# Kernel tuning notes

Measured on AMD Instinct MI355X. Metric: run time of the kernel, lower is better.

The kernel has to match this reference:

```python
import jax, jax.numpy as jnp
import numpy as np

B, S, D = 4, 2048, 1024          # batch, seq, hidden_units
E, K, I = 16, 2, 1024            # n_routed_experts, top_k, moe_inter_dim
SH = 2                            # n_shared_experts -> shared inter = SH*I
ROUTE_SCALE = 1.0


def setup_inputs() -> dict:
    key = jax.random.key(0)
    ks = jax.random.split(key, 12)
    std = 0.02
    return {
        "x": jax.random.normal(ks[0], (B, S, D), jnp.float32),
        "gate_w": jax.random.normal(ks[1], (E, D), jnp.float32) * std,
        # expert weights, torch Linear layout [out, in], stacked over experts
        "w1": jax.random.normal(ks[2], (E, I, D), jnp.float32) * std,
        "w2": jax.random.normal(ks[3], (E, D, I), jnp.float32) * std,
        "w3": jax.random.normal(ks[4], (E, I, D), jnp.float32) * std,
        # shared expert MLP (bias=True, nn.Linear default)
        "sw1": jax.random.normal(ks[5], (SH * I, D), jnp.float32) * std,
        "sb1": jnp.zeros((SH * I,), jnp.float32),
        "sw2": jax.random.normal(ks[6], (D, SH * I), jnp.float32) * std,
        "sb2": jnp.zeros((D,), jnp.float32),
        "sw3": jax.random.normal(ks[7], (SH * I, D), jnp.float32) * std,
        "sb3": jnp.zeros((SH * I,), jnp.float32),
    }


def reference(x, gate_w, w1, w2, w3, sw1, sb1, sw2, sb2, sw3, sb3):
    orig_shape = x.shape
    xt = x.reshape(-1, D)                       # [T, D]
    T = xt.shape[0]

    # ---- Gate: sigmoid scores, top-k, normalized weights ----
    scores = jax.nn.sigmoid(xt @ gate_w.T)      # [T, E]
    topk_vals, topk_idx = jax.lax.top_k(scores, K)
    weights = topk_vals / topk_vals.sum(-1, keepdims=True) * ROUTE_SCALE  # [T, K]

    # dense per-token-per-expert combine weight (zero for unselected experts)
    onehot = jax.nn.one_hot(topk_idx, E, dtype=xt.dtype)  # [T, K, E]
    w_full = jnp.einsum('tk,tke->te', weights, onehot)    # [T, E]

    # ---- Routed experts: SwiGLU per expert, weighted combine ----
    y = jnp.zeros_like(xt)
    for e in range(E):  # fixed small structural loop over experts
        h = jax.nn.silu(xt @ w1[e].T) * (xt @ w3[e].T)    # [T, I]
        y = y + w_full[:, e:e + 1] * (h @ w2[e].T)

    # ---- Load-balancing auxiliary loss ----
    counts = jax.lax.stop_gradient(onehot.sum((0, 1)))    # tokens per expert (non-diff, as in torch)
    expert_probs = w_full.sum(0)                          # sum of routing weights per expert
    f_i = E * counts / (K * T)
    P_i = expert_probs / T
    L_ExpBal = (f_i * P_i).sum()

    # ---- Shared expert (dense SwiGLU MLP with bias) ----
    z = (jax.nn.silu(xt @ sw1.T + sb1) * (xt @ sw3.T + sb3)) @ sw2.T + sb2

    return (y + z).reshape(orig_shape), L_ExpBal
```

## Files before the change

kernel.cpp:

```cpp
#include <hip/hip_runtime.h>
#include <cstdint>
#include <cstddef>

typedef unsigned short ushort_t;
typedef __attribute__((ext_vector_type(8))) short bf16x8;
typedef __attribute__((ext_vector_type(8))) unsigned short u16x8;
typedef __attribute__((ext_vector_type(4))) float f32x4;

#define T_TOKENS 8192
#define DIM      1024
#define NEXP     16

static __device__ __forceinline__ unsigned short f2bf(float f) {
  union { float f; unsigned u; } v; v.f = f;
  unsigned r = v.u + 0x7FFFu + ((v.u >> 16) & 1u);
  return (unsigned short)(r >> 16);
}

static __device__ __forceinline__ void gload16(const void* g, void* l) {
  __builtin_amdgcn_global_load_lds(
      (const __attribute__((address_space(1))) unsigned int*)g,
      (__attribute__((address_space(3))) unsigned int*)l, 16, 0, 0);
}

static __device__ __forceinline__ void xcd_map(int bx, int by, int gy,
                                               int& rb, int& cb) {
  int lin = bx + (by << 6);
  int xcd = lin & 7;
  int c = lin >> 3;
  int gyd = gy >> 3;
  cb = xcd * gyd + (c >> 6);
  rb = c & 63;
}

__global__ __launch_bounds__(256) void k_cvt_score(
    const float* __restrict__ x,  const float* __restrict__ w1,
    const float* __restrict__ w2, const float* __restrict__ w3,
    const float* __restrict__ sw1, const float* __restrict__ sw2,
    const float* __restrict__ sw3, const float* __restrict__ gw,
    ushort_t* __restrict__ xb,  ushort_t* __restrict__ w1b,
    ushort_t* __restrict__ w2b, ushort_t* __restrict__ w3b,
    ushort_t* __restrict__ sw1b, ushort_t* __restrict__ sw2b,
    ushort_t* __restrict__ sw3b,
    int* __restrict__ sel0, int* __restrict__ sel1,
    float* __restrict__ w0o, float* __restrict__ w1o) {
  int b = blockIdx.x;
  if (b >= 31744) {
    int lane = threadIdx.x & 63;
    int wv = threadIdx.x >> 6;
    int t = (b - 31744) * 4 + wv;
    float xv[16];
    const float* xr = x + (size_t)t * DIM + lane * 16;
#pragma unroll
    for (int j = 0; j < 16; j += 4) {
      float4 v = *(const float4*)(xr + j);
      xv[j] = v.x; xv[j+1] = v.y; xv[j+2] = v.z; xv[j+3] = v.w;
    }
    float sc[NEXP];
#pragma unroll
    for (int e = 0; e < NEXP; e++) {
      const float* gr = gw + (size_t)e * DIM + lane * 16;
      float a = 0.f;
#pragma unroll
      for (int j = 0; j < 16; j += 4) {
        float4 g = *(const float4*)(gr + j);
        a += xv[j]*g.x + xv[j+1]*g.y + xv[j+2]*g.z + xv[j+3]*g.w;
      }
#pragma unroll
      for (int o = 32; o > 0; o >>= 1) a += __shfl_xor(a, o, 64);
      sc[e] = 1.f / (1.f + expf(-a));
    }
    if (lane == 0) {
      float best = -1e30f, sec = -1e30f;
      int bi = 0, si = 0;
#pragma unroll
      for (int e = 0; e < NEXP; e++) {
        float s = sc[e];
        if (s > best) { sec = best; si = bi; best = s; bi = e; }
        else if (s > sec) { sec = s; si = e; }
      }
      float inv = 1.f / (best + sec);
      sel0[t] = bi; sel1[t] = si;
      w0o[t] = best * inv; w1o[t] = sec * inv;
    }
    return;
  }
  const float* src; ushort_t* dst; int rel;
  if (b < 4096)       { src = x;   dst = xb;   rel = b; }
  else if (b < 12288) { src = w1;  dst = w1b;  rel = b - 4096; }
  else if (b < 20480) { src = w2;  dst = w2b;  rel = b - 12288; }
  else if (b < 28672) { src = w3;  dst = w3b;  rel = b - 20480; }
  else if (b < 29696) { src = sw1; dst = sw1b; rel = b - 28672; }
  else if (b < 30720) { src = sw2; dst = sw2b; rel = b - 29696; }
  else                { src = sw3; dst = sw3b; rel = b - 30720; }
  size_t i = ((size_t)rel * 256 + threadIdx.x) * 8;
  float4 a = *(const float4*)(src + i);
  float4 c = *(const float4*)(src + i + 4);
  u16x8 o;
  o[0]=f2bf(a.x); o[1]=f2bf(a.y); o[2]=f2bf(a.z); o[3]=f2bf(a.w);
  o[4]=f2bf(c.x); o[5]=f2bf(c.y); o[6]=f2bf(c.z); o[7]=f2bf(c.w);
  *(u16x8*)(dst + i) = o;
}

__global__ __launch_bounds__(256) void k_compact(const int* __restrict__ sel0,
                                                 const int* __restrict__ sel1,
                                                 const float* __restrict__ w0v,
                                                 const float* __restrict__ w1v,
                                                 int* __restrict__ toklist,
                                                 float* __restrict__ wlist,
                                                 int* __restrict__ cnt,
                                                 float* __restrict__ probs) {
  const int e = blockIdx.x;
  const int tid = threadIdx.x;
  const int lane = tid & 63, wv = tid >> 6;
  __shared__ int wbase[4];
  __shared__ int woff[4];
  __shared__ int base;
  __shared__ float pacc[4];
  if (tid == 0) base = 0;
  float myprob = 0.f;
  int* tl = toklist + e * T_TOKENS;
  float* wl = wlist + e * T_TOKENS;
  __syncthreads();
  for (int t0 = 0; t0 < T_TOKENS; t0 += 256) {
    int t = t0 + tid;
    bool m0 = (sel0[t] == e), m1 = (sel1[t] == e);
    bool m = m0 || m1;
    float wgt = m0 ? w0v[t] : (m1 ? w1v[t] : 0.f);
    unsigned long long bal = __ballot(m);
    int prefix = __popcll(bal & ((1ull << lane) - 1ull));
    if (lane == 0) wbase[wv] = __popcll(bal);
    __syncthreads();
    if (tid == 0) {
      int a = base;
#pragma unroll
      for (int i = 0; i < 4; i++) { woff[i] = a; a += wbase[i]; }
      base = a;
    }
    __syncthreads();
    if (m) {
      int pos = woff[wv] + prefix;
      tl[pos] = t;
      wl[pos] = wgt;
    }
    myprob += wgt;
  }
#pragma unroll
  for (int o = 32; o > 0; o >>= 1) myprob += __shfl_xor(myprob, o, 64);
  if (lane == 0) pacc[wv] = myprob;
  __syncthreads();
  if (tid == 0) {
    cnt[e] = base;
    probs[e] = pacc[0] + pacc[1] + pacc[2] + pacc[3];
  }
}

__global__ void k_offsets(const int* __restrict__ cnt, const float* __restrict__ probs,
                          int* __restrict__ seg, float* __restrict__ loss_out) {
  if (threadIdx.x == 0 && blockIdx.x == 0) {
    int acc = 0;
    float L = 0.f;
    for (int e = 0; e < NEXP; e++) {
      seg[e] = acc; acc += cnt[e];
      float f = 16.f * (float)cnt[e] / (2.f * 8192.f);
      L += f * (probs[e] / 8192.f);
    }
    seg[NEXP] = acc;
    *loss_out = L;
  }
}


__global__ __launch_bounds__(256, 4) void k_gemm1(
    const ushort_t* __restrict__ X,
    const ushort_t* __restrict__ w1b, const ushort_t* __restrict__ w3b,
    const ushort_t* __restrict__ sw1b, const ushort_t* __restrict__ sw3b,
    const float* __restrict__ sb1, const float* __restrict__ sb3,
    ushort_t* __restrict__ Pr, ushort_t* __restrict__ Ps,
    const int* __restrict__ toklist, const int* __restrict__ cnt,
    const int* __restrict__ seg, int zbase) {
  __shared__ __align__(16) ushort_t As[8192];
  __shared__ __align__(16) ushort_t B1s[4096];
  __shared__ __align__(16) ushort_t B3s[4096];

  const int tid = threadIdx.x;
  const int lane = tid & 63, wave = tid >> 6;
  const int wm = wave >> 1, wn = wave & 1;
  const int e = blockIdx.z + zbase;

  int rb, cb, Ne, pbase, ldP;
  const int* tl = nullptr;
  const ushort_t *W1, *W3;
  const float *b1 = nullptr, *b3 = nullptr;
  ushort_t* P;
  if (e < NEXP) {
    if (blockIdx.y >= 16) return;
    xcd_map(blockIdx.x, blockIdx.y, 16, rb, cb);
    Ne = cnt[e];
    if (rb * 128 >= Ne) return;
    pbase = seg[e];
    tl = toklist + e * T_TOKENS;
    W1 = w1b + (size_t)e * 1024 * 1024;
    W3 = w3b + (size_t)e * 1024 * 1024;
    P = Pr; ldP = 1024;
  } else {
    xcd_map(blockIdx.x, blockIdx.y, 32, rb, cb);
    Ne = T_TOKENS; pbase = 0;
    W1 = sw1b; W3 = sw3b; b1 = sb1; b3 = sb3;
    P = Ps; ldP = 2048;
  }

  const int lrow = lane >> 3;
  const int scol = ((lane & 7) ^ lrow) * 8;

  const int ca = wave * 4;
  int ga0 = rb * 128 + (ca + 0) * 8 + lrow;
  int ga1 = rb * 128 + (ca + 1) * 8 + lrow;
  int ga2 = rb * 128 + (ca + 2) * 8 + lrow;
  int ga3 = rb * 128 + (ca + 3) * 8 + lrow;
  const int s0 = tl ? tl[min(ga0, Ne - 1)] : ga0;
  const int s1 = tl ? tl[min(ga1, Ne - 1)] : ga1;
  const int s2 = tl ? tl[min(ga2, Ne - 1)] : ga2;
  const int s3 = tl ? tl[min(ga3, Ne - 1)] : ga3;
  const ushort_t* apA0 = X + (size_t)s0 * DIM + scol;
  const ushort_t* apA1 = X + (size_t)s1 * DIM + scol;
  const ushort_t* apA2 = X + (size_t)s2 * DIM + scol;
  const ushort_t* apA3 = X + (size_t)s3 * DIM + scol;
  const int oa0 = (ca + 0) * 512, oa1 = (ca + 1) * 512;
  const int oa2 = (ca + 2) * 512, oa3 = (ca + 3) * 512;

  const int brw0 = cb * 64 + wave * 16 + lrow;
  const int brw1 = brw0 + 8;
  const ushort_t* bp10 = W1 + (size_t)brw0 * DIM + scol;
  const ushort_t* bp11 = W1 + (size_t)brw1 * DIM + scol;
  const ushort_t* bp30 = W3 + (size_t)brw0 * DIM + scol;
  const ushort_t* bp31 = W3 + (size_t)brw1 * DIM + scol;
  const int ob0 = (wave * 2) * 512, ob1 = (wave * 2 + 1) * 512;

  const int ks0 = (((lane >> 4) + 0) ^ (lane & 7)) * 8;
  const int ks1 = (((lane >> 4) + 4) ^ (lane & 7)) * 8;

  f32x4 acc1[4][2], acc3[4][2];
#pragma unroll
  for (int m = 0; m < 4; m++)
#pragma unroll
    for (int n = 0; n < 2; n++) {
      acc1[m][n] = (f32x4){0.f, 0.f, 0.f, 0.f};
      acc3[m][n] = (f32x4){0.f, 0.f, 0.f, 0.f};
    }

#define HALF1(KS) { \
    bf16x8 af[4], b1f[2], b3f[2]; \
    _Pragma("unroll") \
    for (int m = 0; m < 4; m++) { \
      int row = wm * 64 + m * 16 + (lane & 15); \
      af[m] = *(const bf16x8*)(As + row * 64 + (KS)); } \
    _Pragma("unroll") \
    for (int n = 0; n < 2; n++) { \
      int rw = wn * 32 + n * 16 + (lane & 15); \
      b1f[n] = *(const bf16x8*)(B1s + rw * 64 + (KS)); \
      b3f[n] = *(const bf16x8*)(B3s + rw * 64 + (KS)); } \
    _Pragma("unroll") \
    for (int m = 0; m < 4; m++) \
      _Pragma("unroll") \
      for (int n = 0; n < 2; n++) { \
        acc1[m][n] = __builtin_amdgcn_mfma_f32_16x16x32_bf16(af[m], b1f[n], acc1[m][n], 0, 0, 0); \
        acc3[m][n] = __builtin_amdgcn_mfma_f32_16x16x32_bf16(af[m], b3f[n], acc3[m][n], 0, 0, 0); } }

  for (int t = 0; t < 16; ++t) {
    const int k0 = t * 64;
    gload16(apA0 + k0, As  + oa0);
    gload16(apA1 + k0, As  + oa1);
    gload16(apA2 + k0, As  + oa2);
    gload16(apA3 + k0, As  + oa3);
    gload16(bp10 + k0, B1s + ob0);
    gload16(bp11 + k0, B1s + ob1);
    gload16(bp30 + k0, B3s + ob0);
    gload16(bp31 + k0, B3s + ob1);
    __syncthreads();
    HALF1(ks0);
    HALF1(ks1);
    __syncthreads();
  }
#undef HALF1

#pragma unroll
  for (int n = 0; n < 2; n++) {
    int col = cb * 64 + wn * 32 + n * 16 + (lane & 15);
    float bb1 = b1 ? b1[col] : 0.f;
    float bb3 = b3 ? b3[col] : 0.f;
#pragma unroll
    for (int m = 0; m < 4; m++) {
#pragma unroll
      for (int r = 0; r < 4; r++) {
        int row = rb * 128 + wm * 64 + m * 16 + (lane >> 4) * 4 + r;
        if (row < Ne) {
          float h1 = acc1[m][n][r] + bb1;
          float h3 = acc3[m][n][r] + bb3;
          float pv = (h1 / (1.f + expf(-h1))) * h3;
          P[(size_t)(pbase + row) * ldP + col] = f2bf(pv);
        }
      }
    }
  }
}

__global__ __launch_bounds__(256, 4) void k_gemm2(
    const ushort_t* __restrict__ Pr, const ushort_t* __restrict__ Ps,
    const ushort_t* __restrict__ w2b, const ushort_t* __restrict__ sw2b,
    const float* __restrict__ sb2,
    float* __restrict__ outp,
    const int* __restrict__ toklist, const float* __restrict__ wlist,
    const int* __restrict__ cnt, const int* __restrict__ seg, int zbase) {
  __shared__ __align__(16) ushort_t As[8192];
  __shared__ __align__(16) ushort_t Bs[8192];

  const int tid = threadIdx.x;
  const int lane = tid & 63, wave = tid >> 6;
  const int wm = wave >> 1, wn = wave & 1;
  const int e = blockIdx.z + zbase;
  int rb, cb;
  xcd_map(blockIdx.x, blockIdx.y, 8, rb, cb);

  int Ne, Kd;
  const ushort_t *A, *W2;
  const int* tl = nullptr; const float* wl = nullptr;
  const float* b2 = nullptr;
  if (e < NEXP) {
    Ne = cnt[e];
    if (rb * 128 >= Ne) return;
    A = Pr + (size_t)seg[e] * 1024;
    W2 = w2b + (size_t)e * 1024 * 1024;
    tl = toklist + e * T_TOKENS;
    wl = wlist + e * T_TOKENS;
    Kd = 1024;
  } else {
    Ne = T_TOKENS;
    A = Ps; W2 = sw2b; b2 = sb2; Kd = 2048;
  }

  const int lrow = lane >> 3;
  const int scol = ((lane & 7) ^ lrow) * 8;

  const int ca = wave * 4;
  const int a0 = min(rb * 128 + (ca + 0) * 8 + lrow, Ne - 1);
  const int a1 = min(rb * 128 + (ca + 1) * 8 + lrow, Ne - 1);
  const int a2 = min(rb * 128 + (ca + 2) * 8 + lrow, Ne - 1);
  const int a3 = min(rb * 128 + (ca + 3) * 8 + lrow, Ne - 1);
  const ushort_t* apA0 = A + (size_t)a0 * Kd + scol;
  const ushort_t* apA1 = A + (size_t)a1 * Kd + scol;
  const ushort_t* apA2 = A + (size_t)a2 * Kd + scol;
  const ushort_t* apA3 = A + (size_t)a3 * Kd + scol;
  const int oa0 = (ca + 0) * 512, oa1 = (ca + 1) * 512;
  const int oa2 = (ca + 2) * 512, oa3 = (ca + 3) * 512;

  const int br0 = cb * 128 + (ca + 0) * 8 + lrow;
  const int br1 = cb * 128 + (ca + 1) * 8 + lrow;
  const int br2 = cb * 128 + (ca + 2) * 8 + lrow;
  const int br3 = cb * 128 + (ca + 3) * 8 + lrow;
  const ushort_t* bp0 = W2 + (size_t)br0 * Kd + scol;
  const ushort_t* bp1 = W2 + (size_t)br1 * Kd + scol;
  const ushort_t* bp2 = W2 + (size_t)br2 * Kd + scol;
  const ushort_t* bp3 = W2 + (size_t)br3 * Kd + scol;

  const int ks0 = (((lane >> 4) + 0) ^ (lane & 7)) * 8;
  const int ks1 = (((lane >> 4) + 4) ^ (lane & 7)) * 8;

  f32x4 acc[4][4];
#pragma unroll
  for (int m = 0; m < 4; m++)
#pragma unroll
    for (int n = 0; n < 4; n++) acc[m][n] = (f32x4){0.f, 0.f, 0.f, 0.f};

  const int ksteps = Kd >> 6;

#define HALF2(KS) { \
    bf16x8 af[4], bf[4]; \
    _Pragma("unroll") \
    for (int m = 0; m < 4; m++) { \
      int row = wm * 64 + m * 16 + (lane & 15); \
      af[m] = *(const bf16x8*)(As + row * 64 + (KS)); } \
    _Pragma("unroll") \
    for (int n = 0; n < 4; n++) { \
      int rw = wn * 64 + n * 16 + (lane & 15); \
      bf[n] = *(const bf16x8*)(Bs + rw * 64 + (KS)); } \
    _Pragma("unroll") \
    for (int m = 0; m < 4; m++) \
      _Pragma("unroll") \
      for (int n = 0; n < 4; n++) \
        acc[m][n] = __builtin_amdgcn_mfma_f32_16x16x32_bf16(af[m], bf[n], acc[m][n], 0, 0, 0); }

  for (int t = 0; t < ksteps; ++t) {
    const int k0 = t * 64;
    gload16(apA0 + k0, As + oa0);
    gload16(apA1 + k0, As + oa1);
    gload16(apA2 + k0, As + oa2);
    gload16(apA3 + k0, As + oa3);
    gload16(bp0  + k0, Bs + oa0);
    gload16(bp1  + k0, Bs + oa1);
    gload16(bp2  + k0, Bs + oa2);
    gload16(bp3  + k0, Bs + oa3);
    __syncthreads();
    HALF2(ks0);
    HALF2(ks1);
    __syncthreads();
  }
#undef HALF2

#pragma unroll
  for (int n = 0; n < 4; n++) {
    int col = cb * 128 + wn * 64 + n * 16 + (lane & 15);
    float bias = b2 ? b2[col] : 0.f;
#pragma unroll
    for (int m = 0; m < 4; m++) {
#pragma unroll
      for (int r = 0; r < 4; r++) {
        int rl = rb * 128 + wm * 64 + m * 16 + (lane >> 4) * 4 + r;
        if (e < NEXP) {
          if (rl < Ne) {
            int tok = tl[rl];
            float wgt = wl[rl];
            atomicAdd(outp + (size_t)tok * DIM + col, acc[m][n][r] * wgt);
          }
        } else {
          atomicAdd(outp + (size_t)rl * DIM + col, acc[m][n][r] + bias);
        }
      }
    }
  }
}

extern "C" void kernel_launch(void* const* d_in, const int* in_sizes, int n_in,
                              void* d_out, int out_size, void* d_ws, size_t ws_size,
                              hipStream_t stream) {
  const float* x   = (const float*)d_in[0];
  const float* gw  = (const float*)d_in[1];
  const float* w1  = (const float*)d_in[2];
  const float* w2  = (const float*)d_in[3];
  const float* w3  = (const float*)d_in[4];
  const float* sw1 = (const float*)d_in[5];
  const float* sb1 = (const float*)d_in[6];
  const float* sw2 = (const float*)d_in[7];
  const float* sb2 = (const float*)d_in[8];
  const float* sw3 = (const float*)d_in[9];
  const float* sb3 = (const float*)d_in[10];
  float* out  = (float*)d_out;
  float* loss = out + (size_t)T_TOKENS * DIM;

  const size_t NW = (size_t)NEXP * 1024 * 1024;
  const size_t NS = (size_t)2048 * 1024;
  const size_t PSZ = (size_t)16384 * 1024 * 2;

  char* w = (char*)d_ws;
  ushort_t* w1b  = (ushort_t*)w; w += NW * 2;
  ushort_t* w2b  = (ushort_t*)w; w += NW * 2;
  ushort_t* w3b  = (ushort_t*)w; w += NW * 2;
  ushort_t* sw1b = (ushort_t*)w; w += NS * 2;
  ushort_t* sw2b = (ushort_t*)w; w += NS * 2;
  ushort_t* sw3b = (ushort_t*)w; w += NS * 2;
  ushort_t* Pr   = (ushort_t*)w; w += PSZ;
  ushort_t* x_bf = (ushort_t*)w; w += (size_t)T_TOKENS * DIM * 2;
  int*   toklist = (int*)w;      w += (size_t)NEXP * T_TOKENS * 4;
  float* wlist   = (float*)w;    w += (size_t)NEXP * T_TOKENS * 4;
  int*   sel0    = (int*)w;      w += (size_t)T_TOKENS * 4;
  int*   sel1    = (int*)w;      w += (size_t)T_TOKENS * 4;
  float* w0v     = (float*)w;    w += (size_t)T_TOKENS * 4;
  float* w1v     = (float*)w;    w += (size_t)T_TOKENS * 4;
  int*   cnt     = (int*)w;      w += 64;
  float* probs   = (float*)w;    w += 64;
  int*   seg     = (int*)w;      w += 128;

  size_t used = (size_t)(w - (char*)d_ws);
  bool fused = (used + PSZ + 1024) <= ws_size;
  ushort_t* Ps = fused ? (ushort_t*)w : Pr;

  hipMemsetAsync(d_out, 0, (size_t)out_size * 4, stream);

  k_cvt_score<<<33792, 256, 0, stream>>>(x, w1, w2, w3, sw1, sw2, sw3, gw,
                                         x_bf, w1b, w2b, w3b, sw1b, sw2b, sw3b,
                                         sel0, sel1, w0v, w1v);

  k_compact<<<NEXP, 256, 0, stream>>>(sel0, sel1, w0v, w1v,
                                      toklist, wlist, cnt, probs);
  k_offsets<<<1, 64, 0, stream>>>(cnt, probs, seg, loss);

  if (fused) {
    k_gemm1<<<dim3(64, 32, 17), 256, 0, stream>>>(
        x_bf, w1b, w3b, sw1b, sw3b, sb1, sb3, Pr, Ps,
        toklist, cnt, seg, 0);
    k_gemm2<<<dim3(64, 8, 17), 256, 0, stream>>>(
        Pr, Ps, w2b, sw2b, sb2, out, toklist, wlist, cnt, seg, 0);
  } else {
    k_gemm1<<<dim3(64, 32, 1), 256, 0, stream>>>(
        x_bf, w1b, w3b, sw1b, sw3b, sb1, sb3, Pr, Ps,
        toklist, cnt, seg, 16);
    k_gemm2<<<dim3(64, 8, 1), 256, 0, stream>>>(
        Pr, Ps, w2b, sw2b, sb2, out, toklist, wlist, cnt, seg, 16);
    k_gemm1<<<dim3(64, 16, 16), 256, 0, stream>>>(
        x_bf, w1b, w3b, sw1b, sw3b, sb1, sb3, Pr, Ps,
        toklist, cnt, seg, 0);
    k_gemm2<<<dim3(64, 8, 16), 256, 0, stream>>>(
        Pr, Ps, w2b, sw2b, sb2, out, toklist, wlist, cnt, seg, 0);
  }
}
```

Measured before the change: 492.2 us.

## Register-prefetch GEMM tiles and write shared-expert output directly instead of memset+atomics

```diff
diff --git a/kernel.cpp b/kernel.cpp
--- a/kernel.cpp
+++ b/kernel.cpp
@@ -15,12 +15,6 @@
   union { float f; unsigned u; } v; v.f = f;
   unsigned r = v.u + 0x7FFFu + ((v.u >> 16) & 1u);
   return (unsigned short)(r >> 16);
-}
-
-static __device__ __forceinline__ void gload16(const void* g, void* l) {
-  __builtin_amdgcn_global_load_lds(
-      (const __attribute__((address_space(1))) unsigned int*)g,
-      (__attribute__((address_space(3))) unsigned int*)l, 16, 0, 0);
 }
 
 static __device__ __forceinline__ void xcd_map(int bx, int by, int gy,
@@ -171,7 +165,7 @@
 }
 
 
-__global__ __launch_bounds__(256, 4) void k_gemm1(
+__global__ __launch_bounds__(256, 3) void k_gemm1(
     const ushort_t* __restrict__ X,
     const ushort_t* __restrict__ w1b, const ushort_t* __restrict__ w3b,
     const ushort_t* __restrict__ sw1b, const ushort_t* __restrict__ sw3b,
@@ -226,8 +220,11 @@
   const ushort_t* apA1 = X + (size_t)s1 * DIM + scol;
   const ushort_t* apA2 = X + (size_t)s2 * DIM + scol;
   const ushort_t* apA3 = X + (size_t)s3 * DIM + scol;
-  const int oa0 = (ca + 0) * 512, oa1 = (ca + 1) * 512;
-  const int oa2 = (ca + 2) * 512, oa3 = (ca + 3) * 512;
+  const int la8 = lane << 3;
+  ushort_t* dA0 = As + (ca + 0) * 512 + la8;
+  ushort_t* dA1 = As + (ca + 1) * 512 + la8;
+  ushort_t* dA2 = As + (ca + 2) * 512 + la8;
+  ushort_t* dA3 = As + (ca + 3) * 512 + la8;
 
   const int brw0 = cb * 64 + wave * 16 + lrow;
   const int brw1 = brw0 + 8;
@@ -235,7 +232,10 @@
   const ushort_t* bp11 = W1 + (size_t)brw1 * DIM + scol;
   const ushort_t* bp30 = W3 + (size_t)brw0 * DIM + scol;
   const ushort_t* bp31 = W3 + (size_t)brw1 * DIM + scol;
-  const int ob0 = (wave * 2) * 512, ob1 = (wave * 2 + 1) * 512;
+  ushort_t* dB10 = B1s + (wave * 2 + 0) * 512 + la8;
+  ushort_t* dB11 = B1s + (wave * 2 + 1) * 512 + la8;
+  ushort_t* dB30 = B3s + (wave * 2 + 0) * 512 + la8;
+  ushort_t* dB31 = B3s + (wave * 2 + 1) * 512 + la8;
 
   const int ks0 = (((lane >> 4) + 0) ^ (lane & 7)) * 8;
   const int ks1 = (((lane >> 4) + 4) ^ (lane & 7)) * 8;
@@ -248,6 +248,28 @@
       acc1[m][n] = (f32x4){0.f, 0.f, 0.f, 0.f};
       acc3[m][n] = (f32x4){0.f, 0.f, 0.f, 0.f};
     }
+
+  bf16x8 rA0, rA1, rA2, rA3, rB10, rB11, rB30, rB31;
+
+#define LOAD1(K0) { \
+    rA0  = *(const bf16x8*)(apA0 + (K0)); \
+    rA1  = *(const bf16x8*)(apA1 + (K0)); \
+    rA2  = *(const bf16x8*)(apA2 + (K0)); \
+    rA3  = *(const bf16x8*)(apA3 + (K0)); \
+    rB10 = *(const bf16x8*)(bp10 + (K0)); \
+    rB11 = *(const bf16x8*)(bp11 + (K0)); \
+    rB30 = *(const bf16x8*)(bp30 + (K0)); \
+    rB31 = *(const bf16x8*)(bp31 + (K0)); }
+
+#define WRITE1() { \
+    *(bf16x8*)dA0  = rA0; \
+    *(bf16x8*)dA1  = rA1; \
+    *(bf16x8*)dA2  = rA2; \
+    *(bf16x8*)dA3  = rA3; \
+    *(bf16x8*)dB10 = rB10; \
+    *(bf16x8*)dB11 = rB11; \
+    *(bf16x8*)dB30 = rB30; \
+    *(bf16x8*)dB31 = rB31; }
 
 #define HALF1(KS) { \
     bf16x8 af[4], b1f[2], b3f[2]; \
@@ -267,22 +289,21 @@
         acc1[m][n] = __builtin_amdgcn_mfma_f32_16x16x32_bf16(af[m], b1f[n], acc1[m][n], 0, 0, 0); \
         acc3[m][n] = __builtin_amdgcn_mfma_f32_16x16x32_bf16(af[m], b3f[n], acc3[m][n], 0, 0, 0); } }
 
+  LOAD1(0);
+  WRITE1();
+  __syncthreads();
+
   for (int t = 0; t < 16; ++t) {
-    const int k0 = t * 64;
-    gload16(apA0 + k0, As  + oa0);
-    gload16(apA1 + k0, As  + oa1);
-    gload16(apA2 + k0, As  + oa2);
-    gload16(apA3 + k0, As  + oa3);
-    gload16(bp10 + k0, B1s + ob0);
-    gload16(bp11 + k0, B1s + ob1);
-    gload16(bp30 + k0, B3s + ob0);
-    gload16(bp31 + k0, B3s + ob1);
-    __syncthreads();
+    if (t < 15) LOAD1((t + 1) * 64);
     HALF1(ks0);
     HALF1(ks1);
     __syncthreads();
+    if (t < 15) WRITE1();
+    __syncthreads();
   }
 #undef HALF1
+#undef WRITE1
+#undef LOAD1
 
 #pragma unroll
   for (int n = 0; n < 2; n++) {
@@ -305,7 +326,7 @@
   }
 }
 
-__global__ __launch_bounds__(256, 4) void k_gemm2(
+__global__ __launch_bounds__(256, 3) void k_gemm2(
     const ushort_t* __restrict__ Pr, const ushort_t* __restrict__ Ps,
     const ushort_t* __restrict__ w2b, const ushort_t* __restrict__ sw2b,
     const float* __restrict__ sb2,
@@ -351,8 +372,11 @@
   const ushort_t* apA1 = A + (size_t)a1 * Kd + scol;
   const ushort_t* apA2 = A + (size_t)a2 * Kd + scol;
   const ushort_t* apA3 = A + (size_t)a3 * Kd + scol;
-  const int oa0 = (ca + 0) * 512, oa1 = (ca + 1) * 512;
-  const int oa2 = (ca + 2) * 512, oa3 = (ca + 3) * 512;
+  const int la8 = lane << 3;
+  ushort_t* dA0 = As + (ca + 0) * 512 + la8;
+  ushort_t* dA1 = As + (ca + 1) * 512 + la8;
+  ushort_t* dA2 = As + (ca + 2) * 512 + la8;
+  ushort_t* dA3 = As + (ca + 3) * 512 + la8;
 
   const int br0 = cb * 128 + (ca + 0) * 8 + lrow;
   const int br1 = cb * 128 + (ca + 1) * 8 + lrow;
@@ -362,6 +386,10 @@
   const ushort_t* bp1 = W2 + (size_t)br1 * Kd + scol;
   const ushort_t* bp2 = W2 + (size_t)br2 * Kd + scol;
   const ushort_t* bp3 = W2 + (size_t)br3 * Kd + scol;
+  ushort_t* dB0 = Bs + (ca + 0) * 512 + la8;
+  ushort_t* dB1 = Bs + (ca + 1) * 512 + la8;
+  ushort_t* dB2 = Bs + (ca + 2) * 512 + la8;
+  ushort_t* dB3 = Bs + (ca + 3) * 512 + la8;
 
   const int ks0 = (((lane >> 4) + 0) ^ (lane & 7)) * 8;
   const int ks1 = (((lane >> 4) + 4) ^ (lane & 7)) * 8;
@@ -373,6 +401,28 @@
     for (int n = 0; n < 4; n++) acc[m][n] = (f32x4){0.f, 0.f, 0.f, 0.f};
 
   const int ksteps = Kd >> 6;
+
+  bf16x8 rA0, rA1, rA2, rA3, rB0, rB1, rB2, rB3;
+
+#define LOAD2(K0) { \
+    rA0 = *(const bf16x8*)(apA0 + (K0)); \
+    rA1 = *(const bf16x8*)(apA1 + (K0)); \
+    rA2 = *(const bf16x8*)(apA2 + (K0)); \
+    rA3 = *(const bf16x8*)(apA3 + (K0)); \
+    rB0 = *(const bf16x8*)(bp0 + (K0)); \
+    rB1 = *(const bf16x8*)(bp1 + (K0)); \
+    rB2 = *(const bf16x8*)(bp2 + (K0)); \
+    rB3 = *(const bf16x8*)(bp3 + (K0)); }
+
+#define WRITE2() { \
+    *(bf16x8*)dA0 = rA0; \
+    *(bf16x8*)dA1 = rA1; \
+    *(bf16x8*)dA2 = rA2; \
+    *(bf16x8*)dA3 = rA3; \
+    *(bf16x8*)dB0 = rB0; \
+    *(bf16x8*)dB1 = rB1; \
+    *(bf16x8*)dB2 = rB2; \
+    *(bf16x8*)dB3 = rB3; }
 
 #define HALF2(KS) { \
     bf16x8 af[4], bf[4]; \
@@ -390,22 +440,21 @@
       for (int n = 0; n < 4; n++) \
         acc[m][n] = __builtin_amdgcn_mfma_f32_16x16x32_bf16(af[m], bf[n], acc[m][n], 0, 0, 0); }
 
+  LOAD2(0);
+  WRITE2();
+  __syncthreads();
+
   for (int t = 0; t < ksteps; ++t) {
-    const int k0 = t * 64;
-    gload16(apA0 + k0, As + oa0);
-    gload16(apA1 + k0, As + oa1);
-    gload16(apA2 + k0, As + oa2);
-    gload16(apA3 + k0, As + oa3);
-    gload16(bp0  + k0, Bs + oa0);
-    gload16(bp1  + k0, Bs + oa1);
-    gload16(bp2  + k0, Bs + oa2);
-    gload16(bp3  + k0, Bs + oa3);
-    __syncthreads();
+    if (t < ksteps - 1) LOAD2((t + 1) * 64);
     HALF2(ks0);
     HALF2(ks1);
     __syncthreads();
+    if (t < ksteps - 1) WRITE2();
+    __syncthreads();
   }
 #undef HALF2
+#undef WRITE2
+#undef LOAD2
 
 #pragma unroll
   for (int n = 0; n < 4; n++) {
@@ -423,7 +472,7 @@
             atomicAdd(outp + (size_t)tok * DIM + col, acc[m][n][r] * wgt);
           }
         } else {
-          atomicAdd(outp + (size_t)rl * DIM + col, acc[m][n][r] + bias);
+          outp[(size_t)rl * DIM + col] = acc[m][n][r] + bias;
         }
       }
     }
@@ -474,8 +523,6 @@
   bool fused = (used + PSZ + 1024) <= ws_size;
   ushort_t* Ps = fused ? (ushort_t*)w : Pr;
 
-  hipMemsetAsync(d_out, 0, (size_t)out_size * 4, stream);
-
   k_cvt_score<<<33792, 256, 0, stream>>>(x, w1, w2, w3, sw1, sw2, sw3, gw,
                                          x_bf, w1b, w2b, w3b, sw1b, sw2b, sw3b,
                                          sel0, sel1, w0v, w1v);
@@ -488,7 +535,9 @@
     k_gemm1<<<dim3(64, 32, 17), 256, 0, stream>>>(
         x_bf, w1b, w3b, sw1b, sw3b, sb1, sb3, Pr, Ps,
         toklist, cnt, seg, 0);
-    k_gemm2<<<dim3(64, 8, 17), 256, 0, stream>>>(
+    k_gemm2<<<dim3(64, 8, 1), 256, 0, stream>>>(
+        Pr, Ps, w2b, sw2b, sb2, out, toklist, wlist, cnt, seg, 16);
+    k_gemm2<<<dim3(64, 8, 16), 256, 0, stream>>>(
         Pr, Ps, w2b, sw2b, sb2, out, toklist, wlist, cnt, seg, 0);
   } else {
     k_gemm1<<<dim3(64, 32, 1), 256, 0, stream>>>(
```

Result: no change. 495.9 us (+0.8%).
